# Kernel tuning notes

Hardware: AMD Instinct MI355X
Metric: run time of the kernel (lower is better)

Reference implementation:

```python
import jax, jax.numpy as jnp
import numpy as np

NUM_DAYOFWEEK, NUM_TIME, NUM_MONTH, NUM_DAY = 7, 24, 12, 31
NUM_DESTINATION = 100000
NUM_FACTOR = 128
NUM_DIM = NUM_FACTOR // 4  # 32
N = 1048576


def setup_inputs() -> dict:
    key = jax.random.key(0)
    ks = jax.random.split(key, 10)
    std = 0.1
    return {
        "dayofweek": jax.random.randint(ks[0], (N,), 0, NUM_DAYOFWEEK),
        "time": jax.random.randint(ks[1], (N,), 0, NUM_TIME),
        "month": jax.random.randint(ks[2], (N,), 0, NUM_MONTH),
        "day": jax.random.randint(ks[3], (N,), 0, NUM_DAY),
        "destination": jax.random.randint(ks[4], (N,), 0, NUM_DESTINATION),
        "W_dayofweek": std * jax.random.normal(ks[5], (NUM_DAYOFWEEK, NUM_DIM), dtype=jnp.float32),
        "W_time": std * jax.random.normal(ks[6], (NUM_TIME, NUM_DIM), dtype=jnp.float32),
        "W_month": std * jax.random.normal(ks[7], (NUM_MONTH, NUM_DIM), dtype=jnp.float32),
        "W_day": std * jax.random.normal(ks[8], (NUM_DAY, NUM_DIM), dtype=jnp.float32),
        "W_item": std * jax.random.normal(ks[9], (NUM_DESTINATION, NUM_FACTOR), dtype=jnp.float32),
    }


def reference(dayofweek, time, month, day, destination,
              W_dayofweek, W_time, W_month, W_day, W_item) -> jnp.ndarray:
    # Gather per-feature embeddings and concat into user vector [N, num_factor]
    user = jnp.concatenate([
        W_dayofweek[dayofweek],  # [N, 32]
        W_time[time],            # [N, 32]
        W_month[month],          # [N, 32]
        W_day[day],              # [N, 32]
    ], axis=-1)
    item = W_item[destination]   # [N, 128]
    # Original: diagonal(mm(user, item.T)) == rowwise dot product; compute it directly.
    return jnp.sum(user * item, axis=-1)  # [N]
```

## Files before the change

kernel.cpp:

```cpp
#include <hip/hip_runtime.h>


constexpr int NDIM = 32;
constexpr int SZ_DOW = 7 * NDIM, SZ_TIM = 24 * NDIM, SZ_MON = 12 * NDIM, SZ_DAY = 31 * NDIM;
constexpr int B_DOW = 0;
constexpr int B_TIM = B_DOW + SZ_DOW;
constexpr int B_MON = B_TIM + SZ_TIM;
constexpr int B_DAY = B_MON + SZ_MON;
constexpr int TAB_TOT = B_DAY + SZ_DAY;

constexpr int NB    = 32;
constexpr int DDIV  = 3125;
constexpr int NBLK  = 256;
constexpr int SPB   = 4096;
constexpr int BIN_T = 1024;
constexpr int IPT   = SPB / BIN_T;

typedef unsigned long long u64;

__device__ __forceinline__ void load_tab(float* tab, const float* Wdow, const float* Wtim,
                                         const float* Wmon, const float* Wday, int nthr) {
    const int t = threadIdx.x;
    for (int i = t; i < SZ_DOW; i += nthr) tab[B_DOW + i] = Wdow[i];
    for (int i = t; i < SZ_TIM; i += nthr) tab[B_TIM + i] = Wtim[i];
    for (int i = t; i < SZ_MON; i += nthr) tab[B_MON + i] = Wmon[i];
    for (int i = t; i < SZ_DAY; i += nthr) tab[B_DAY + i] = Wday[i];
}

__global__ __launch_bounds__(BIN_T)
void bin_kernel(const int* __restrict__ dow, const int* __restrict__ tim,
                const int* __restrict__ mon, const int* __restrict__ day,
                const int* __restrict__ dest,
                int* __restrict__ cntG, int* __restrict__ lbaseG,
                u64* __restrict__ payload, unsigned short* __restrict__ invl, int n)
{
    __shared__ u64 stage[SPB];
    __shared__ unsigned short ist[SPB];
    __shared__ int hist[NB], lbase[NB], cursor[NB];

    const int t = threadIdx.x, b = blockIdx.x;
    const int g0 = b * SPB;
    const int rem = n - g0;
    const int len = rem < SPB ? rem : SPB;

    int dreg[IPT], pkreg[IPT];
#pragma unroll
    for (int i = 0; i < IPT; i++) {
        const int k = i * BIN_T + t;
        if (k < len) {
            const int idx = g0 + k;
            dreg[i]  = dest[idx];
            pkreg[i] = dow[idx] | (tim[idx] << 3) | (mon[idx] << 8) | (day[idx] << 12);
        } else { dreg[i] = -1; pkreg[i] = 0; }
    }
    if (t < NB) hist[t] = 0;
    __syncthreads();
#pragma unroll
    for (int i = 0; i < IPT; i++)
        if (dreg[i] >= 0) atomicAdd(&hist[dreg[i] / DDIV], 1);
    __syncthreads();
    if (t == 0) {
        int run = 0;
        for (int q = 0; q < NB; q++) { lbase[q] = run; run += hist[q]; }
    }
    __syncthreads();
    if (t < NB) { cursor[t] = lbase[t]; cntG[b * NB + t] = hist[t]; lbaseG[b * NB + t] = lbase[t]; }
    __syncthreads();
#pragma unroll
    for (int i = 0; i < IPT; i++) {
        const int k = i * BIN_T + t;
        if (k < len) {
            const int ds = dreg[i];
            const int j  = atomicAdd(&cursor[ds / DDIV], 1);
            stage[j] = (u64)(unsigned)(g0 + k)
                     | ((u64)(unsigned)ds       << 20)
                     | ((u64)(unsigned)pkreg[i] << 37);
            ist[k] = (unsigned short)j;
        }
    }
    __syncthreads();
#pragma unroll
    for (int i = 0; i < IPT; i++) {
        const int k = i * BIN_T + t;
        if (k < len) {
            payload[g0 + k] = stage[k];
            invl[g0 + k]    = ist[k];
        }
    }
}

__global__ __launch_bounds__(256, 8)
void mf_main_kernel(const u64* __restrict__ payload,
                    const float* __restrict__ Wdow, const float* __restrict__ Wtim,
                    const float* __restrict__ Wmon, const float* __restrict__ Wday,
                    const float* __restrict__ Witem,
                    const int* __restrict__ cntG, const int* __restrict__ lbaseG,
                    float* __restrict__ res)
{
    __shared__ float tab[TAB_TOT];
    load_tab(tab, Wdow, Wtim, Wmon, Wday, 256);
    __syncthreads();

    const int tid = threadIdx.x;
    const int sub = tid & 63;
    const int wv  = tid >> 6;
    const int g   = sub >> 3;
    const int l8  = sub & 7;
    const int col = l8 * 4;
    const int tb[4] = {B_DOW, B_TIM, B_MON, B_DAY};
    const int sh[4] = {37, 40, 45, 49};
    const int mk[4] = {7, 31, 15, 31};

    const int x = blockIdx.x & 7;
    const int s = blockIdx.x >> 3;

    int Ls[4], sts[4];
#pragma unroll
    for (int p = 0; p < 4; p++) {
        const int q = x + 8 * p;
        Ls[p]  = cntG[s * NB + q];
        sts[p] = s * SPB + lbaseG[s * NB + q];
    }

#pragma unroll
    for (int p = 0; p < 4; p++) {
        const int L  = Ls[p];
        const int st = sts[p];

        for (int i = wv * 16; i < L; i += 64) {
            const int i0 = i + g, i1 = i + 8 + g;
            const bool v0 = i0 < L, v1 = i1 < L;

            const u64 p0 = v0 ? payload[st + i0] : 0ull;
            const u64 p1 = v1 ? payload[st + i1] : 0ull;

            const int d0 = (int)((p0 >> 20) & 0x1FFFFull);
            const int d1 = (int)((p1 >> 20) & 0x1FFFFull);

            const float* r0 = Witem + (long)d0 * 128 + col;
            const float* r1 = Witem + (long)d1 * 128 + col;

            float4 it0[4], it1[4], us0[4], us1[4];
#pragma unroll
            for (int j = 0; j < 4; j++) it0[j] = *reinterpret_cast<const float4*>(r0 + j * NDIM);
#pragma unroll
            for (int j = 0; j < 4; j++) it1[j] = *reinterpret_cast<const float4*>(r1 + j * NDIM);
#pragma unroll
            for (int j = 0; j < 4; j++) {
                const int idx = (int)((p0 >> sh[j]) & (u64)mk[j]);
                us0[j] = *reinterpret_cast<const float4*>(&tab[tb[j] + idx * NDIM + col]);
            }
#pragma unroll
            for (int j = 0; j < 4; j++) {
                const int idx = (int)((p1 >> sh[j]) & (u64)mk[j]);
                us1[j] = *reinterpret_cast<const float4*>(&tab[tb[j] + idx * NDIM + col]);
            }

            float a0 = 0.f, a1 = 0.f;
#pragma unroll
            for (int j = 0; j < 4; j++) {
                a0 += it0[j].x * us0[j].x + it0[j].y * us0[j].y
                    + it0[j].z * us0[j].z + it0[j].w * us0[j].w;
                a1 += it1[j].x * us1[j].x + it1[j].y * us1[j].y
                    + it1[j].z * us1[j].z + it1[j].w * us1[j].w;
            }

            a0 += __shfl_xor(a0, 1);  a1 += __shfl_xor(a1, 1);
            a0 += __shfl_xor(a0, 2);  a1 += __shfl_xor(a1, 2);
            a0 += __shfl_xor(a0, 4);  a1 += __shfl_xor(a1, 4);

            if (l8 == 0) {
                if (v0) res[st + i0] = a0;
                if (v1) res[st + i1] = a1;
            }
        }
    }
}

__global__ __launch_bounds__(BIN_T)
void unperm_kernel(const float* __restrict__ res, const unsigned short* __restrict__ invl,
                   float* __restrict__ out, int n)
{
    __shared__ float r[SPB];
    const int t = threadIdx.x, b = blockIdx.x;
    const int g0 = b * SPB;
    const int rem = n - g0;
    const int len = rem < SPB ? rem : SPB;

    unsigned short iv[IPT];
#pragma unroll
    for (int i = 0; i < IPT; i++) {
        const int k = i * BIN_T + t;
        iv[i] = (k < len) ? invl[g0 + k] : 0;
        if (k < len) r[k] = res[g0 + k];
    }
    __syncthreads();
#pragma unroll
    for (int i = 0; i < IPT; i++) {
        const int k = i * BIN_T + t;
        if (k < len) out[g0 + k] = r[iv[i]];
    }
}

__global__ __launch_bounds__(256, 8)
void mf_dot_kernel(const int* __restrict__ dow, const int* __restrict__ tim,
                   const int* __restrict__ mon, const int* __restrict__ day,
                   const int* __restrict__ dest,
                   const float* __restrict__ Wdow, const float* __restrict__ Wtim,
                   const float* __restrict__ Wmon, const float* __restrict__ Wday,
                   const float* __restrict__ Witem,
                   float* __restrict__ out, int n_samples)
{
    __shared__ float tab[TAB_TOT];
    load_tab(tab, Wdow, Wtim, Wmon, Wday, 256);
    __syncthreads();
    const int tid = threadIdx.x;
    const int lane = tid & 63, sub = lane & 31, wave = tid >> 6, half = lane >> 5;
    const int t = sub >> 3, dofs = (sub & 7) * 4;
    const int* idxp  = (t == 0) ? dow   : (t == 1) ? tim   : (t == 2) ? mon   : day;
    const int  tbase = (t == 0) ? B_DOW : (t == 1) ? B_TIM : (t == 2) ? B_MON : B_DAY;
    long n = (long)blockIdx.x * 8 + wave * 2 + half;
    const long stride = (long)gridDim.x * 8;
    for (; n < n_samples; n += stride) {
        const int idx = idxp[n];
        const int ds  = dest[n];
        const float4 u  = *reinterpret_cast<const float4*>(&tab[tbase + idx * NDIM + dofs]);
        const float4 it = *reinterpret_cast<const float4*>(&Witem[(long)ds * 128 + sub * 4]);
        float r = u.x * it.x + u.y * it.y + u.z * it.z + u.w * it.w;
        r += __shfl_xor(r, 16); r += __shfl_xor(r, 8); r += __shfl_xor(r, 4);
        r += __shfl_xor(r, 2);  r += __shfl_xor(r, 1);
        if (sub == 0) out[n] = r;
    }
}

extern "C" void kernel_launch(void* const* d_in, const int* in_sizes, int n_in,
                              void* d_out, int out_size, void* d_ws, size_t ws_size,
                              hipStream_t stream)
{
    const int*   dow   = (const int*)d_in[0];
    const int*   tim   = (const int*)d_in[1];
    const int*   mon   = (const int*)d_in[2];
    const int*   day   = (const int*)d_in[3];
    const int*   dest  = (const int*)d_in[4];
    const float* Wdow  = (const float*)d_in[5];
    const float* Wtim  = (const float*)d_in[6];
    const float* Wmon  = (const float*)d_in[7];
    const float* Wday  = (const float*)d_in[8];
    const float* Witem = (const float*)d_in[9];
    float* out = (float*)d_out;

    const int n = in_sizes[0];
    const int cap = NBLK * SPB;

    const size_t off_payload = 64 * 1024;
    const size_t off_invl    = off_payload + (size_t)cap * 8;
    const size_t off_res     = off_invl + (size_t)cap * 2;
    const size_t need        = off_res + (size_t)cap * 4;

    if ((size_t)ws_size < need || n > cap) {
        hipLaunchKernelGGL(mf_dot_kernel, dim3(2048), dim3(256), 0, stream,
                           dow, tim, mon, day, dest,
                           Wdow, Wtim, Wmon, Wday, Witem, out, n);
        return;
    }

    int* cntG    = (int*)d_ws;
    int* lbaseG  = (int*)((char*)d_ws + 32 * 1024);
    u64* payload = (u64*)((char*)d_ws + off_payload);
    unsigned short* invl = (unsigned short*)((char*)d_ws + off_invl);
    float* res           = (float*)((char*)d_ws + off_res);

    hipLaunchKernelGGL(bin_kernel, dim3(NBLK), dim3(BIN_T), 0, stream,
                       dow, tim, mon, day, dest, cntG, lbaseG, payload, invl, n);
    hipLaunchKernelGGL(mf_main_kernel, dim3(NBLK * 8), dim3(256), 0, stream,
                       payload, Wdow, Wtim, Wmon, Wday, Witem, cntG, lbaseG, res);
    hipLaunchKernelGGL(unperm_kernel, dim3(NBLK), dim3(BIN_T), 0, stream,
                       res, invl, out, n);
}
```

Measured before the change: 153.9 us.

## Globally sort samples by destination and reuse item rows across consecutive samples

Replaces the per-block 32-bucket binning and the unpermute pass with a global two-level sort by destination. A count, a scan and a scatter put samples into 128 coarse buckets, then a per-chunk counting sort orders them by exact destination. The dot kernel then walks the sorted payload, reloads the W_item row only when the destination changes, and writes each result straight to its original index. This is meant to cut redundant W_item gather traffic and drop the separate unpermute pass. In exchange it adds more kernel launches, a single-block scan, and scattered 4-byte output stores.

```diff
diff --git a/kernel.cpp b/kernel.cpp
--- a/kernel.cpp
+++ b/kernel.cpp
@@ -1,5 +1,7 @@
 #include <hip/hip_runtime.h>
 
+
+typedef unsigned long long u64;
 
 constexpr int NDIM = 32;
 constexpr int SZ_DOW = 7 * NDIM, SZ_TIM = 24 * NDIM, SZ_MON = 12 * NDIM, SZ_DAY = 31 * NDIM;
@@ -9,14 +11,13 @@
 constexpr int B_DAY = B_MON + SZ_MON;
 constexpr int TAB_TOT = B_DAY + SZ_DAY;
 
-constexpr int NB    = 32;
-constexpr int DDIV  = 3125;
-constexpr int NBLK  = 256;
-constexpr int SPB   = 4096;
-constexpr int BIN_T = 1024;
-constexpr int IPT   = SPB / BIN_T;
-
-typedef unsigned long long u64;
+constexpr int NBA    = 128;
+constexpr int DDIVA  = 782;
+constexpr int SLICES = 256;
+constexpr int SPS    = 4096;
+constexpr int AT     = 1024;
+constexpr int AIPT   = SPS / AT;
+constexpr int BKEYS  = 2048;
 
 __device__ __forceinline__ void load_tab(float* tab, const float* Wdow, const float* Wtim,
                                          const float* Wmon, const float* Wday, int nthr) {
@@ -27,75 +28,176 @@
     for (int i = t; i < SZ_DAY; i += nthr) tab[B_DAY + i] = Wday[i];
 }
 
-__global__ __launch_bounds__(BIN_T)
-void bin_kernel(const int* __restrict__ dow, const int* __restrict__ tim,
-                const int* __restrict__ mon, const int* __restrict__ day,
-                const int* __restrict__ dest,
-                int* __restrict__ cntG, int* __restrict__ lbaseG,
-                u64* __restrict__ payload, unsigned short* __restrict__ invl, int n)
-{
-    __shared__ u64 stage[SPB];
-    __shared__ unsigned short ist[SPB];
-    __shared__ int hist[NB], lbase[NB], cursor[NB];
-
+__global__ __launch_bounds__(AT)
+void countA_kernel(const int* __restrict__ dest, int* __restrict__ cntA, int n)
+{
+    __shared__ int h[NBA];
     const int t = threadIdx.x, b = blockIdx.x;
-    const int g0 = b * SPB;
+    const int g0 = b * SPS;
+    int d[AIPT];
+#pragma unroll
+    for (int i = 0; i < AIPT; i++) {
+        const int k = i * AT + t;
+        d[i] = (g0 + k < n) ? dest[g0 + k] : -1;
+    }
+    if (t < NBA) h[t] = 0;
+    __syncthreads();
+#pragma unroll
+    for (int i = 0; i < AIPT; i++)
+        if (d[i] >= 0) atomicAdd(&h[d[i] / DDIVA], 1);
+    __syncthreads();
+    if (t < NBA) cntA[t * SLICES + b] = h[t];
+}
+
+__global__ __launch_bounds__(AT)
+void scanA_kernel(int* __restrict__ cntA)
+{
+    __shared__ int part[AT];
+    const int t = threadIdx.x;
+    const int base = t * 32;
+    int v[32], s = 0;
+#pragma unroll
+    for (int i = 0; i < 32; i++) { v[i] = cntA[base + i]; s += v[i]; }
+    part[t] = s;
+    __syncthreads();
+    for (int off = 1; off < AT; off <<= 1) {
+        const int x = (t >= off) ? part[t - off] : 0;
+        __syncthreads();
+        part[t] += x;
+        __syncthreads();
+    }
+    int run = part[t] - s;
+#pragma unroll
+    for (int i = 0; i < 32; i++) { cntA[base + i] = run; run += v[i]; }
+}
+
+__global__ __launch_bounds__(AT)
+void scatterA_kernel(const int* __restrict__ dow, const int* __restrict__ tim,
+                     const int* __restrict__ mon, const int* __restrict__ day,
+                     const int* __restrict__ dest, const int* __restrict__ offA,
+                     u64* __restrict__ payload, int n)
+{
+    __shared__ u64 stage[SPS];
+    __shared__ int h[NBA], lb[NBA], cur[NBA], offQ[NBA];
+    const int t = threadIdx.x, b = blockIdx.x;
+    const int g0 = b * SPS;
     const int rem = n - g0;
-    const int len = rem < SPB ? rem : SPB;
-
-    int dreg[IPT], pkreg[IPT];
-#pragma unroll
-    for (int i = 0; i < IPT; i++) {
-        const int k = i * BIN_T + t;
+    const int len = rem < SPS ? rem : SPS;
+
+    int dreg[AIPT], pk[AIPT];
+#pragma unroll
+    for (int i = 0; i < AIPT; i++) {
+        const int k = i * AT + t;
         if (k < len) {
             const int idx = g0 + k;
-            dreg[i]  = dest[idx];
-            pkreg[i] = dow[idx] | (tim[idx] << 3) | (mon[idx] << 8) | (day[idx] << 12);
-        } else { dreg[i] = -1; pkreg[i] = 0; }
-    }
-    if (t < NB) hist[t] = 0;
-    __syncthreads();
-#pragma unroll
-    for (int i = 0; i < IPT; i++)
-        if (dreg[i] >= 0) atomicAdd(&hist[dreg[i] / DDIV], 1);
+            dreg[i] = dest[idx];
+            pk[i]   = dow[idx] | (tim[idx] << 3) | (mon[idx] << 8) | (day[idx] << 12);
+        } else { dreg[i] = -1; pk[i] = 0; }
+    }
+    if (t < NBA) h[t] = 0;
+    __syncthreads();
+#pragma unroll
+    for (int i = 0; i < AIPT; i++)
+        if (dreg[i] >= 0) atomicAdd(&h[dreg[i] / DDIVA], 1);
     __syncthreads();
     if (t == 0) {
         int run = 0;
-        for (int q = 0; q < NB; q++) { lbase[q] = run; run += hist[q]; }
-    }
-    __syncthreads();
-    if (t < NB) { cursor[t] = lbase[t]; cntG[b * NB + t] = hist[t]; lbaseG[b * NB + t] = lbase[t]; }
-    __syncthreads();
-#pragma unroll
-    for (int i = 0; i < IPT; i++) {
-        const int k = i * BIN_T + t;
+        for (int q = 0; q < NBA; q++) { lb[q] = run; run += h[q]; }
+    }
+    __syncthreads();
+    if (t < NBA) { cur[t] = lb[t]; offQ[t] = offA[t * SLICES + b]; }
+    __syncthreads();
+#pragma unroll
+    for (int i = 0; i < AIPT; i++) {
+        const int k = i * AT + t;
         if (k < len) {
-            const int ds = dreg[i];
-            const int j  = atomicAdd(&cursor[ds / DDIV], 1);
+            const int j = atomicAdd(&cur[dreg[i] / DDIVA], 1);
             stage[j] = (u64)(unsigned)(g0 + k)
-                     | ((u64)(unsigned)ds       << 20)
-                     | ((u64)(unsigned)pkreg[i] << 37);
-            ist[k] = (unsigned short)j;
+                     | ((u64)(unsigned)dreg[i] << 20)
+                     | ((u64)(unsigned)pk[i]   << 37);
         }
     }
     __syncthreads();
 #pragma unroll
-    for (int i = 0; i < IPT; i++) {
-        const int k = i * BIN_T + t;
+    for (int i = 0; i < AIPT; i++) {
+        const int k = i * AT + t;
         if (k < len) {
-            payload[g0 + k] = stage[k];
-            invl[g0 + k]    = ist[k];
+            const u64 p = stage[k];
+            const int q = (int)((p >> 20) & 0x1FFFFull) / DDIVA;
+            payload[offQ[q] + (k - lb[q])] = p;
         }
     }
 }
 
+__global__ __launch_bounds__(AT)
+void sortB_kernel(u64* __restrict__ payload, int n)
+{
+    __shared__ u64 stage[SPS];
+    __shared__ int h[BKEYS];
+    __shared__ int cur[BKEYS];
+    __shared__ int part[AT];
+    __shared__ int sh_base;
+    const int t = threadIdx.x, b = blockIdx.x;
+    const int w0 = b * SPS;
+    const int rem = n - w0;
+    const int len = rem < SPS ? rem : SPS;
+
+    u64 preg[AIPT]; int key[AIPT];
+#pragma unroll
+    for (int i = 0; i < AIPT; i++) {
+        const int k = i * AT + t;
+        preg[i] = (k < len) ? payload[w0 + k] : 0ull;
+    }
+    if (t == 0)
+        sh_base = ((int)((preg[0] >> 20) & 0x1FFFFull) / DDIVA) * DDIVA;
+    h[t] = 0; h[t + AT] = 0;
+    __syncthreads();
+    const int base = sh_base;
+#pragma unroll
+    for (int i = 0; i < AIPT; i++) {
+        const int k = i * AT + t;
+        if (k < len) {
+            int kk = (int)((preg[i] >> 20) & 0x1FFFFull) - base;
+            kk = kk < 0 ? 0 : (kk > BKEYS - 1 ? BKEYS - 1 : kk);
+            key[i] = kk;
+            atomicAdd(&h[kk], 1);
+        } else key[i] = 0;
+    }
+    __syncthreads();
+    const int a0 = h[2 * t], a1 = h[2 * t + 1];
+    const int s = a0 + a1;
+    part[t] = s;
+    __syncthreads();
+    for (int off = 1; off < AT; off <<= 1) {
+        const int x = (t >= off) ? part[t - off] : 0;
+        __syncthreads();
+        part[t] += x;
+        __syncthreads();
+    }
+    const int e = part[t] - s;
+    h[2 * t] = e; h[2 * t + 1] = e + a0;
+    __syncthreads();
+    cur[2 * t] = h[2 * t]; cur[2 * t + 1] = h[2 * t + 1];
+    __syncthreads();
+#pragma unroll
+    for (int i = 0; i < AIPT; i++) {
+        const int k = i * AT + t;
+        if (k < len) stage[atomicAdd(&cur[key[i]], 1)] = preg[i];
+    }
+    __syncthreads();
+#pragma unroll
+    for (int i = 0; i < AIPT; i++) {
+        const int k = i * AT + t;
+        if (k < len) payload[w0 + k] = stage[k];
+    }
+}
+
 __global__ __launch_bounds__(256, 8)
-void mf_main_kernel(const u64* __restrict__ payload,
-                    const float* __restrict__ Wdow, const float* __restrict__ Wtim,
-                    const float* __restrict__ Wmon, const float* __restrict__ Wday,
-                    const float* __restrict__ Witem,
-                    const int* __restrict__ cntG, const int* __restrict__ lbaseG,
-                    float* __restrict__ res)
+void mf_sorted_kernel(const u64* __restrict__ payload,
+                      const float* __restrict__ Wdow, const float* __restrict__ Wtim,
+                      const float* __restrict__ Wmon, const float* __restrict__ Wday,
+                      const float* __restrict__ Witem,
+                      float* __restrict__ out, int n)
 {
     __shared__ float tab[TAB_TOT];
     load_tab(tab, Wdow, Wtim, Wmon, Wday, 256);
@@ -111,94 +213,39 @@
     const int sh[4] = {37, 40, 45, 49};
     const int mk[4] = {7, 31, 15, 31};
 
-    const int x = blockIdx.x & 7;
-    const int s = blockIdx.x >> 3;
-
-    int Ls[4], sts[4];
-#pragma unroll
-    for (int p = 0; p < 4; p++) {
-        const int q = x + 8 * p;
-        Ls[p]  = cntG[s * NB + q];
-        sts[p] = s * SPB + lbaseG[s * NB + q];
-    }
-
-#pragma unroll
-    for (int p = 0; p < 4; p++) {
-        const int L  = Ls[p];
-        const int st = sts[p];
-
-        for (int i = wv * 16; i < L; i += 64) {
-            const int i0 = i + g, i1 = i + 8 + g;
-            const bool v0 = i0 < L, v1 = i1 < L;
-
-            const u64 p0 = v0 ? payload[st + i0] : 0ull;
-            const u64 p1 = v1 ? payload[st + i1] : 0ull;
-
-            const int d0 = (int)((p0 >> 20) & 0x1FFFFull);
-            const int d1 = (int)((p1 >> 20) & 0x1FFFFull);
-
-            const float* r0 = Witem + (long)d0 * 128 + col;
-            const float* r1 = Witem + (long)d1 * 128 + col;
-
-            float4 it0[4], it1[4], us0[4], us1[4];
-#pragma unroll
-            for (int j = 0; j < 4; j++) it0[j] = *reinterpret_cast<const float4*>(r0 + j * NDIM);
-#pragma unroll
-            for (int j = 0; j < 4; j++) it1[j] = *reinterpret_cast<const float4*>(r1 + j * NDIM);
-#pragma unroll
-            for (int j = 0; j < 4; j++) {
-                const int idx = (int)((p0 >> sh[j]) & (u64)mk[j]);
-                us0[j] = *reinterpret_cast<const float4*>(&tab[tb[j] + idx * NDIM + col]);
-            }
-#pragma unroll
-            for (int j = 0; j < 4; j++) {
-                const int idx = (int)((p1 >> sh[j]) & (u64)mk[j]);
-                us1[j] = *reinterpret_cast<const float4*>(&tab[tb[j] + idx * NDIM + col]);
-            }
-
-            float a0 = 0.f, a1 = 0.f;
-#pragma unroll
-            for (int j = 0; j < 4; j++) {
-                a0 += it0[j].x * us0[j].x + it0[j].y * us0[j].y
-                    + it0[j].z * us0[j].z + it0[j].w * us0[j].w;
-                a1 += it1[j].x * us1[j].x + it1[j].y * us1[j].y
-                    + it1[j].z * us1[j].z + it1[j].w * us1[j].w;
-            }
-
-            a0 += __shfl_xor(a0, 1);  a1 += __shfl_xor(a1, 1);
-            a0 += __shfl_xor(a0, 2);  a1 += __shfl_xor(a1, 2);
-            a0 += __shfl_xor(a0, 4);  a1 += __shfl_xor(a1, 4);
-
-            if (l8 == 0) {
-                if (v0) res[st + i0] = a0;
-                if (v1) res[st + i1] = a1;
-            }
+    const int wbase = blockIdx.x * 512 + wv * 128 + g * 16;
+
+    int dcur = -1;
+    float4 it[4];
+
+    for (int k = 0; k < 16; k++) {
+        const int idx = wbase + k;
+        if (idx >= n) break;
+        const u64 p = payload[idx];
+        const int d = (int)((p >> 20) & 0x1FFFFull);
+        if (d != dcur) {
+            dcur = d;
+            const float* r = Witem + (long)d * 128 + col;
+#pragma unroll
+            for (int j = 0; j < 4; j++) it[j] = *reinterpret_cast<const float4*>(r + j * NDIM);
         }
-    }
-}
-
-__global__ __launch_bounds__(BIN_T)
-void unperm_kernel(const float* __restrict__ res, const unsigned short* __restrict__ invl,
-                   float* __restrict__ out, int n)
-{
-    __shared__ float r[SPB];
-    const int t = threadIdx.x, b = blockIdx.x;
-    const int g0 = b * SPB;
-    const int rem = n - g0;
-    const int len = rem < SPB ? rem : SPB;
-
-    unsigned short iv[IPT];
-#pragma unroll
-    for (int i = 0; i < IPT; i++) {
-        const int k = i * BIN_T + t;
-        iv[i] = (k < len) ? invl[g0 + k] : 0;
-        if (k < len) r[k] = res[g0 + k];
-    }
-    __syncthreads();
-#pragma unroll
-    for (int i = 0; i < IPT; i++) {
-        const int k = i * BIN_T + t;
-        if (k < len) out[g0 + k] = r[iv[i]];
+        float4 us[4];
+#pragma unroll
+        for (int j = 0; j < 4; j++) {
+            const int ix = (int)((p >> sh[j]) & (u64)mk[j]);
+            us[j] = *reinterpret_cast<const float4*>(&tab[tb[j] + ix * NDIM + col]);
+        }
+        float a = 0.f;
+#pragma unroll
+        for (int j = 0; j < 4; j++)
+            a += it[j].x * us[j].x + it[j].y * us[j].y
+               + it[j].z * us[j].z + it[j].w * us[j].w;
+
+        a += __shfl_xor(a, 1);
+        a += __shfl_xor(a, 2);
+        a += __shfl_xor(a, 4);
+
+        if (l8 == 0) out[(int)(p & 0xFFFFFull)] = a;
     }
 }
 
@@ -250,12 +297,10 @@
     float* out = (float*)d_out;
 
     const int n = in_sizes[0];
-    const int cap = NBLK * SPB;
-
-    const size_t off_payload = 64 * 1024;
-    const size_t off_invl    = off_payload + (size_t)cap * 8;
-    const size_t off_res     = off_invl + (size_t)cap * 2;
-    const size_t need        = off_res + (size_t)cap * 4;
+    const int cap = SLICES * SPS;
+
+    const size_t off_payload = 128 * 1024;
+    const size_t need = off_payload + (size_t)cap * 8;
 
     if ((size_t)ws_size < need || n > cap) {
         hipLaunchKernelGGL(mf_dot_kernel, dim3(2048), dim3(256), 0, stream,
@@ -264,16 +309,14 @@
         return;
     }
 
-    int* cntG    = (int*)d_ws;
-    int* lbaseG  = (int*)((char*)d_ws + 32 * 1024);
+    int* cntA    = (int*)d_ws;
     u64* payload = (u64*)((char*)d_ws + off_payload);
-    unsigned short* invl = (unsigned short*)((char*)d_ws + off_invl);
-    float* res           = (float*)((char*)d_ws + off_res);
-
-    hipLaunchKernelGGL(bin_kernel, dim3(NBLK), dim3(BIN_T), 0, stream,
-                       dow, tim, mon, day, dest, cntG, lbaseG, payload, invl, n);
-    hipLaunchKernelGGL(mf_main_kernel, dim3(NBLK * 8), dim3(256), 0, stream,
-                       payload, Wdow, Wtim, Wmon, Wday, Witem, cntG, lbaseG, res);
-    hipLaunchKernelGGL(unperm_kernel, dim3(NBLK), dim3(BIN_T), 0, stream,
-                       res, invl, out, n);
-}
+
+    hipLaunchKernelGGL(countA_kernel,   dim3(SLICES), dim3(AT), 0, stream, dest, cntA, n);
+    hipLaunchKernelGGL(scanA_kernel,    dim3(1),      dim3(AT), 0, stream, cntA);
+    hipLaunchKernelGGL(scatterA_kernel, dim3(SLICES), dim3(AT), 0, stream,
+                       dow, tim, mon, day, dest, cntA, payload, n);
+    hipLaunchKernelGGL(sortB_kernel,    dim3(SLICES), dim3(AT), 0, stream, payload, n);
+    hipLaunchKernelGGL(mf_sorted_kernel, dim3((n + 511) / 512), dim3(256), 0, stream,
+                       payload, Wdow, Wtim, Wmon, Wday, Witem, out, n);
+}
```

After: 181.4 us. 1.18x slower.
